# Optimization experiments

Hardware: AMD Instinct MI355X
Metric: run time of the kernel (lower is better)

## Reference

```python
import math
import jax, jax.numpy as jnp
import numpy as np

B, T, C, FD, K, V = 8, 2048, 256, 256, 128, 256

def setup_inputs() -> dict:
    key = jax.random.key(0)
    ks = jax.random.split(key, 8)
    s = 0.02
    return {
        "inp": jax.random.normal(ks[0], (B, T, C), jnp.float32),
        "feature": jax.random.normal(ks[1], (B, T, FD), jnp.float32),
        "Wq": jax.random.normal(ks[2], (C + FD, K), jnp.float32) * s,
        "bq": jnp.zeros((K,), jnp.float32),
        "Wk": jax.random.normal(ks[3], (C, K), jnp.float32) * s,
        "bk": jnp.zeros((K,), jnp.float32),
        "Wv": jax.random.normal(ks[4], (C, V), jnp.float32) * s,
        "bv": jnp.zeros((V,), jnp.float32),
    }

def reference(inp, feature, Wq, bq, Wk, bk, Wv, bv):
    # inp: [B,T,C], feature: [B,T,FD]
    t = inp.shape[1]
    q = jnp.concatenate([inp, feature], axis=-1) @ Wq + bq   # [B,T,K]
    k = inp @ Wk + bk                                        # [B,T,K]
    v = inp @ Wv + bv                                        # [B,T,V]
    # scores[b, j, i] = q_j . k_i ; original masks where i > j (strict upper tri)
    scores = jnp.einsum('bjk,bik->bji', q, k)                # [B,T,T]
    mask = jnp.triu(jnp.ones((t, t), dtype=bool), k=1)       # mask[j,i] = i > j
    scores = jnp.where(mask[None], -jnp.inf, scores) / math.sqrt(K)
    # NOTE: original softmax is over dim=1 (the query/row axis), not the key axis
    attn = jax.nn.softmax(scores, axis=1)                    # [B,T,T]
    out = jnp.einsum('bji,biv->bjv', attn, v)                # [B,T,V]
    return jnp.concatenate([inp, out], axis=-1)              # [B,T,C+V]
```

## Files before the change

### kernel.cpp

```cpp
#include <hip/hip_runtime.h>
#include <hip/hip_bf16.h>
#include <cstdint>

#define Bb  8
#define Tt  2048
#define Cc  256
#define FDd 256
#define Kk  128
#define Vv  256
#define BT  (Bb * Tt)
#define NTRI 136

#define INV_SQRT_K 0.08838834764831845f

typedef __bf16 bf16x8 __attribute__((ext_vector_type(8)));
typedef __bf16 bf16x4 __attribute__((ext_vector_type(4)));
typedef float  f32x4  __attribute__((ext_vector_type(4)));

__device__ __forceinline__ void gload16(const void* g, void* l) {
  __builtin_amdgcn_global_load_lds(
      (const __attribute__((address_space(1))) void*)g,
      (__attribute__((address_space(3))) void*)l, 16, 0, 0);
}

__global__ __launch_bounds__(256) void prep_kernel(
    const float4* __restrict__ inp4, const float4* __restrict__ feat4,
    float4* __restrict__ out4, bf16x4* __restrict__ inpB4,
    bf16x4* __restrict__ featB4)
{
  const int g = blockIdx.x * 256 + threadIdx.x;
  const int row = g >> 6, c = g & 63;
  const float4 x = inp4[g];
  out4[(size_t)row * 128 + c] = x;
  bf16x4 xb; xb[0] = (__bf16)x.x; xb[1] = (__bf16)x.y; xb[2] = (__bf16)x.z; xb[3] = (__bf16)x.w;
  inpB4[g] = xb;
  const float4 f = feat4[g];
  bf16x4 fb; fb[0] = (__bf16)f.x; fb[1] = (__bf16)f.y; fb[2] = (__bf16)f.z; fb[3] = (__bf16)f.w;
  featB4[g] = fb;
}

__global__ __launch_bounds__(256) void wprep_kernel(
    const float* __restrict__ Wq, const float* __restrict__ Wk,
    const float* __restrict__ Wv, __bf16* __restrict__ Wqt,
    __bf16* __restrict__ Wkt, __bf16* __restrict__ Wvt)
{
  const int g = blockIdx.x * 256 + threadIdx.x;
  if (g < 65536) {
    const int n = g >> 9, k = g & 511;
    Wqt[g] = (__bf16)Wq[k * 128 + n];
  } else if (g < 98304) {
    const int h = g - 65536;
    const int n = h >> 8, k = h & 255;
    Wkt[h] = (__bf16)Wk[k * 128 + n];
  } else {
    const int h = g - 98304;
    const int n = h >> 8, k = h & 255;
    Wvt[h] = (__bf16)Wv[k * 256 + n];
  }
}

__global__ __launch_bounds__(256, 3) void qkv_mfma_kernel(
    const __bf16* __restrict__ inpB, const __bf16* __restrict__ featB,
    const __bf16* __restrict__ Wqt, const __bf16* __restrict__ Wkt,
    const __bf16* __restrict__ Wvt,
    const float* __restrict__ bq, const float* __restrict__ bk,
    const float* __restrict__ bv,
    __bf16* __restrict__ qb, __bf16* __restrict__ kb, __bf16* __restrict__ vT)
{
  __shared__ __bf16 Atile[128 * 64];
  __shared__ __bf16 Btile[128 * 64];
  const int panel = blockIdx.y;
  const int m0 = blockIdx.x * 128;
  const int lane = threadIdx.x & 63, wave = threadIdx.x >> 6;
  const int cl = lane & 15, quad = lane >> 4;
  const int jl0 = (wave >> 1) * 64;
  const int vl0 = (wave & 1) * 64;

  const __bf16* Wt; const float* bias; int kblocks;
  if (panel == 0)      { Wt = Wqt; bias = bq; kblocks = 8; }
  else if (panel == 1) { Wt = Wkt; bias = bk; kblocks = 4; }
  else                 { Wt = Wvt + (size_t)(panel - 2) * 128 * 256;
                         bias = bv + (panel - 2) * 128; kblocks = 4; }
  const int Kd = kblocks * 64;

  const int lrow = lane >> 3;
  const int lchunk = ((lane & 7) ^ lrow) * 8;

  f32x4 acc[4][4];
#pragma unroll
  for (int mt = 0; mt < 4; ++mt)
#pragma unroll
    for (int nt = 0; nt < 4; ++nt) acc[mt][nt] = (f32x4){0.f, 0.f, 0.f, 0.f};

  for (int kb = 0; kb < kblocks; ++kb) {
    const __bf16* Asrc = (panel == 0 && kb >= 4) ? featB : inpB;
    const int koff = (panel == 0 && kb >= 4) ? (kb - 4) * 64 : kb * 64;
    __syncthreads();
#pragma unroll
    for (int t = 0; t < 4; ++t) {
      const int r0 = wave * 32 + t * 8;
      gload16(Asrc + (size_t)(m0 + r0 + lrow) * 256 + koff + lchunk, Atile + r0 * 64);
      gload16(Wt + (size_t)(r0 + lrow) * Kd + kb * 64 + lchunk, Btile + r0 * 64);
    }
    __syncthreads();
#pragma unroll
    for (int ks = 0; ks < 2; ++ks) {
      bf16x8 af[4], bfr[4];
#pragma unroll
      for (int mt = 0; mt < 4; ++mt) {
        const int jlr = jl0 + mt * 16 + cl;
        af[mt] = *(const bf16x8*)(Atile + jlr * 64 + (((ks * 4 + quad) ^ (jlr & 7)) * 8));
      }
#pragma unroll
      for (int nt = 0; nt < 4; ++nt) {
        const int vlr = vl0 + nt * 16 + cl;
        bfr[nt] = *(const bf16x8*)(Btile + vlr * 64 + (((ks * 4 + quad) ^ (vlr & 7)) * 8));
      }
#pragma unroll
      for (int mt = 0; mt < 4; ++mt)
#pragma unroll
        for (int nt = 0; nt < 4; ++nt)
          acc[mt][nt] = __builtin_amdgcn_mfma_f32_16x16x32_bf16(af[mt], bfr[nt], acc[mt][nt], 0, 0, 0);
    }
  }

  if (panel < 2) {
    __bf16* dst = (panel == 0) ? qb : kb;
    const float scale = (panel == 0) ? INV_SQRT_K : 1.0f;
#pragma unroll
    for (int mt = 0; mt < 4; ++mt) {
      const int row = m0 + jl0 + mt * 16 + quad * 4;
#pragma unroll
      for (int nt = 0; nt < 4; ++nt) {
        const int col = vl0 + nt * 16 + cl;
        const float bs = bias[col];
#pragma unroll
        for (int r = 0; r < 4; ++r)
          dst[(size_t)(row + r) * Kk + col] = (__bf16)((acc[mt][nt][r] + bs) * scale);
      }
    }
  } else {
    const int b = m0 >> 11;
#pragma unroll
    for (int mt = 0; mt < 4; ++mt) {
      const int t0 = (m0 & (Tt - 1)) + jl0 + mt * 16 + quad * 4;
#pragma unroll
      for (int nt = 0; nt < 4; ++nt) {
        const int vcol = (panel - 2) * 128 + vl0 + nt * 16 + cl;
        const float bs = bias[vl0 + nt * 16 + cl];
        bf16x4 v4;
#pragma unroll
        for (int r = 0; r < 4; ++r) v4[r] = (__bf16)(acc[mt][nt][r] + bs);
        *(bf16x4*)(vT + (size_t)(b * Vv + vcol) * Tt + t0) = v4;
      }
    }
  }
}

__global__ __launch_bounds__(256, 2) void sexp_kernel(
    const __bf16* __restrict__ qb, const __bf16* __restrict__ kb,
    __bf16* __restrict__ expS, float* __restrict__ partialD)
{
  __shared__ __bf16 tiles[2 * 128 * 128];
  __shared__ float lcs[4][64];
  __bf16* Qtile = tiles;
  __bf16* Ktile = tiles + 128 * 128;
  float*  P     = (float*)tiles;

  const int b = blockIdx.y, l = blockIdx.x;
  int jt = 0, base = 0;
  while (base + jt + 1 <= l) { base += jt + 1; ++jt; }
  const int it = l - base;

  const int lane = threadIdx.x & 63, wave = threadIdx.x >> 6;
  const int cl = lane & 15, quad = lane >> 4;
  const int jl0 = (wave >> 1) * 64;
  const int il0 = (wave & 1) * 64;
  const size_t rowbase = (size_t)b * Tt;

  {
    const int srow = lane >> 4;
    const int cslot = lane & 15;
    const __bf16* qsrc = qb + (rowbase + jt * 128) * Kk;
    const __bf16* ksrc = kb + (rowbase + it * 128) * Kk;
#pragma unroll
    for (int t = 0; t < 8; ++t) {
      const int r0 = wave * 32 + t * 4;
      const int row = r0 + srow;
      const int cg = (cslot ^ (row & 7)) * 8;
      gload16(qsrc + (size_t)row * Kk + cg, Qtile + r0 * 128);
      gload16(ksrc + (size_t)row * Kk + cg, Ktile + r0 * 128);
    }
  }
  __syncthreads();

  f32x4 acc[4][4];
#pragma unroll
  for (int mt = 0; mt < 4; ++mt)
#pragma unroll
    for (int nt = 0; nt < 4; ++nt) acc[mt][nt] = (f32x4){0.f, 0.f, 0.f, 0.f};

#pragma unroll
  for (int s = 0; s < 4; ++s) {
    bf16x8 af[4], bfr[4];
#pragma unroll
    for (int mt = 0; mt < 4; ++mt) {
      const int jlr = jl0 + mt * 16 + cl;
      af[mt] = *(const bf16x8*)(Qtile + jlr * 128 + (((s * 4 + quad) ^ (jlr & 7)) * 8));
    }
#pragma unroll
    for (int nt = 0; nt < 4; ++nt) {
      const int ilr = il0 + nt * 16 + cl;
      bfr[nt] = *(const bf16x8*)(Ktile + ilr * 128 + (((s * 4 + quad) ^ (ilr & 7)) * 8));
    }
#pragma unroll
    for (int mt = 0; mt < 4; ++mt)
#pragma unroll
      for (int nt = 0; nt < 4; ++nt)
        acc[mt][nt] = __builtin_amdgcn_mfma_f32_16x16x32_bf16(af[mt], bfr[nt], acc[mt][nt], 0, 0, 0);
  }
  __syncthreads();

  const bool diag = (it == jt);
  float cs[4] = {0.f, 0.f, 0.f, 0.f};
#pragma unroll
  for (int mt = 0; mt < 4; ++mt) {
    const int jl = jl0 + mt * 16 + quad * 4;
#pragma unroll
    for (int nt = 0; nt < 4; ++nt) {
      const int il = il0 + nt * 16 + cl;
#pragma unroll
      for (int r = 0; r < 4; ++r) {
        float p = __expf(acc[mt][nt][r]);
        if (diag && il > (jl + r)) p = 0.f;
        cs[nt] += (float)(__bf16)p;
        P[(jl + r) * 128 + il] = p;
      }
    }
  }
#pragma unroll
  for (int nt = 0; nt < 4; ++nt) {
    cs[nt] += __shfl_xor(cs[nt], 16);
    cs[nt] += __shfl_xor(cs[nt], 32);
  }
  if (quad == 0) {
#pragma unroll
    for (int nt = 0; nt < 4; ++nt) lcs[wave][nt * 16 + cl] = cs[nt];
  }
  __syncthreads();

  __bf16* slot = expS + ((size_t)(b * NTRI + l)) * (128 * 128);
  {
    const int srow = lane >> 4;
    const int c0 = (lane & 15) * 8;
#pragma unroll
    for (int t = 0; t < 8; ++t) {
      const int row = wave * 32 + t * 4 + srow;
      const f32x4 p0 = *(const f32x4*)(P + row * 128 + c0);
      const f32x4 p1 = *(const f32x4*)(P + row * 128 + c0 + 4);
      bf16x8 pb;
#pragma unroll
      for (int u = 0; u < 4; ++u) { pb[u] = (__bf16)p0[u]; pb[4 + u] = (__bf16)p1[u]; }
      *(bf16x8*)(slot + (size_t)row * 128 + c0) = pb;
    }
  }

  const int tid = threadIdx.x;
  if (tid < 128) {
    const int w0 = (tid < 64) ? 0 : 1;
    const int lc = tid & 63;
    const float s = lcs[w0][lc] + lcs[w0 + 2][lc];
    partialD[((size_t)b * 16 + jt) * Tt + it * 128 + tid] = s;
  }
}

__global__ __launch_bounds__(256) void dreduce_kernel(
    const float* __restrict__ partialD, float* __restrict__ recipD)
{
  const int g = blockIdx.x * 256 + threadIdx.x;
  const int b = g >> 11, i = g & (Tt - 1);
  float s = 0.f;
#pragma unroll
  for (int jt = 0; jt < 16; ++jt) s += partialD[((size_t)b * 16 + jt) * Tt + i];
  recipD[g] = 1.0f / s;
}

__global__ __launch_bounds__(256) void vscale_kernel(
    bf16x8* __restrict__ vT8, const float* __restrict__ recipD)
{
  const int g = blockIdx.x * 256 + threadIdx.x;
  const size_t e0 = (size_t)g * 8;
  const int i = (int)(e0 & (Tt - 1));
  const int b = (int)(e0 >> 19);
  bf16x8 v = vT8[g];
  const f32x4 r0 = *(const f32x4*)(recipD + (size_t)b * Tt + i);
  const f32x4 r1 = *(const f32x4*)(recipD + (size_t)b * Tt + i + 4);
#pragma unroll
  for (int t = 0; t < 4; ++t) v[t] = (__bf16)((float)v[t] * r0[t]);
#pragma unroll
  for (int t = 0; t < 4; ++t) v[4 + t] = (__bf16)((float)v[4 + t] * r1[t]);
  vT8[g] = v;
}

__global__ __launch_bounds__(256, 3) void pvgemm_kernel(
    const __bf16* __restrict__ expS, const __bf16* __restrict__ vT,
    float* __restrict__ out)
{
  __shared__ __bf16 Atile[128 * 64];
  __shared__ __bf16 Btile[128 * 64];
  const int b = blockIdx.y;
  const int jt = 15 - (blockIdx.x >> 1);
  const int nh = blockIdx.x & 1;
  const int lane = threadIdx.x & 63, wave = threadIdx.x >> 6;
  const int cl = lane & 15, quad = lane >> 4;
  const int jl0 = (wave >> 1) * 64;
  const int vl0 = (wave & 1) * 64;

  const int kblocks = (jt + 1) * 2;
  const size_t slotbase = (size_t)(b * NTRI + (jt * (jt + 1)) / 2) * 16384;
  const __bf16* vbase = vT + ((size_t)b * Vv + nh * 128) * Tt;

  const int lrow = lane >> 3;
  const int lchunk = ((lane & 7) ^ lrow) * 8;

  f32x4 acc[4][4];
#pragma unroll
  for (int mt = 0; mt < 4; ++mt)
#pragma unroll
    for (int nt = 0; nt < 4; ++nt) acc[mt][nt] = (f32x4){0.f, 0.f, 0.f, 0.f};

  for (int kb = 0; kb < kblocks; ++kb) {
    const int i0 = kb * 64;
    const __bf16* Ag = expS + slotbase + (size_t)(kb >> 1) * 16384 + (kb & 1) * 64;
    __syncthreads();
#pragma unroll
    for (int t = 0; t < 4; ++t) {
      const int r0 = wave * 32 + t * 8;
      gload16(Ag + (size_t)(r0 + lrow) * 128 + lchunk, Atile + r0 * 64);
      gload16(vbase + (size_t)(r0 + lrow) * Tt + i0 + lchunk, Btile + r0 * 64);
    }
    __syncthreads();
#pragma unroll
    for (int ks = 0; ks < 2; ++ks) {
      bf16x8 af[4], bfr[4];
#pragma unroll
      for (int mt = 0; mt < 4; ++mt) {
        const int jlr = jl0 + mt * 16 + cl;
        af[mt] = *(const bf16x8*)(Atile + jlr * 64 + (((ks * 4 + quad) ^ (jlr & 7)) * 8));
      }
#pragma unroll
      for (int nt = 0; nt < 4; ++nt) {
        const int vlr = vl0 + nt * 16 + cl;
        bfr[nt] = *(const bf16x8*)(Btile + vlr * 64 + (((ks * 4 + quad) ^ (vlr & 7)) * 8));
      }
#pragma unroll
      for (int mt = 0; mt < 4; ++mt)
#pragma unroll
        for (int nt = 0; nt < 4; ++nt)
          acc[mt][nt] = __builtin_amdgcn_mfma_f32_16x16x32_bf16(af[mt], bfr[nt], acc[mt][nt], 0, 0, 0);
    }
  }

  float* orow = out + ((size_t)b * Tt + jt * 128 + jl0) * (size_t)(Cc + Vv)
              + Cc + nh * 128 + vl0;
#pragma unroll
  for (int mt = 0; mt < 4; ++mt)
#pragma unroll
    for (int nt = 0; nt < 4; ++nt)
#pragma unroll
      for (int r = 0; r < 4; ++r)
        orow[(size_t)(mt * 16 + quad * 4 + r) * (Cc + Vv) + nt * 16 + cl] = acc[mt][nt][r];
}

extern "C" void kernel_launch(void* const* d_in, const int* in_sizes, int n_in,
                              void* d_out, int out_size, void* d_ws, size_t ws_size,
                              hipStream_t stream) {
  const float* inp  = (const float*)d_in[0];
  const float* feat = (const float*)d_in[1];
  const float* Wq   = (const float*)d_in[2];
  const float* bq   = (const float*)d_in[3];
  const float* Wk   = (const float*)d_in[4];
  const float* bk   = (const float*)d_in[5];
  const float* Wv   = (const float*)d_in[6];
  const float* bv   = (const float*)d_in[7];
  float* out = (float*)d_out;

  char* ws = (char*)d_ws;
  __bf16* inpB   = (__bf16*)(ws);
  __bf16* featB  = (__bf16*)(ws + (8u << 20));
  __bf16* qb     = (__bf16*)(ws + (16u << 20));
  __bf16* kb     = (__bf16*)(ws + (20u << 20));
  __bf16* vT     = (__bf16*)(ws + (24u << 20));
  __bf16* Wqt    = (__bf16*)(ws + (32u << 20));
  __bf16* Wkt    = (__bf16*)(ws + (32u << 20) + (128u << 10));
  __bf16* Wvt    = (__bf16*)(ws + (32u << 20) + (192u << 10));
  float*  partialD = (float*)(ws + (33u << 20));
  float*  recipD   = (float*)(ws + (35u << 20));
  __bf16* expS     = (__bf16*)(ws + (36u << 20));

  prep_kernel<<<dim3(BT * 64 / 256), 256, 0, stream>>>(
      (const float4*)inp, (const float4*)feat, (float4*)out,
      (bf16x4*)inpB, (bf16x4*)featB);
  wprep_kernel<<<dim3(640), 256, 0, stream>>>(Wq, Wk, Wv, Wqt, Wkt, Wvt);
  qkv_mfma_kernel<<<dim3(BT / 128, 4), 256, 0, stream>>>(
      inpB, featB, Wqt, Wkt, Wvt, bq, bk, bv, qb, kb, vT);
  sexp_kernel<<<dim3(NTRI, Bb), 256, 0, stream>>>(qb, kb, expS, partialD);
  dreduce_kernel<<<dim3(BT / 256), 256, 0, stream>>>(partialD, recipD);
  vscale_kernel<<<dim3(2048), 256, 0, stream>>>((bf16x8*)vT, recipD);
  pvgemm_kernel<<<dim3(32, Bb), 256, 0, stream>>>(expS, vT, out);
}
```

Baseline: 173.0 us.

## Split-K the PV GEMM across two wave groups and merge small launches

The PV GEMM now runs 512 threads per block. Two groups of four waves each take half of the K range into separate LDS buffers, and their partial sums are combined through a shared reduction buffer before the output is written. The prep and weight-transpose kernels are merged into one launch, and the column-sum reduction is fused with the V scaling, removing two launches and the recipD round trip. This targets launch overhead and the load imbalance of the triangular PV work, at the cost of extra LDS (about 96KB per block) and an additional synchronisation and reduction step.

```diff
diff --git a/kernel.cpp b/kernel.cpp
--- a/kernel.cpp
+++ b/kernel.cpp
@@ -23,39 +23,38 @@
       (__attribute__((address_space(3))) void*)l, 16, 0, 0);
 }
 
-__global__ __launch_bounds__(256) void prep_kernel(
+__global__ __launch_bounds__(256) void prepw_kernel(
     const float4* __restrict__ inp4, const float4* __restrict__ feat4,
     float4* __restrict__ out4, bf16x4* __restrict__ inpB4,
-    bf16x4* __restrict__ featB4)
-{
-  const int g = blockIdx.x * 256 + threadIdx.x;
-  const int row = g >> 6, c = g & 63;
-  const float4 x = inp4[g];
-  out4[(size_t)row * 128 + c] = x;
-  bf16x4 xb; xb[0] = (__bf16)x.x; xb[1] = (__bf16)x.y; xb[2] = (__bf16)x.z; xb[3] = (__bf16)x.w;
-  inpB4[g] = xb;
-  const float4 f = feat4[g];
-  bf16x4 fb; fb[0] = (__bf16)f.x; fb[1] = (__bf16)f.y; fb[2] = (__bf16)f.z; fb[3] = (__bf16)f.w;
-  featB4[g] = fb;
-}
-
-__global__ __launch_bounds__(256) void wprep_kernel(
+    bf16x4* __restrict__ featB4,
     const float* __restrict__ Wq, const float* __restrict__ Wk,
     const float* __restrict__ Wv, __bf16* __restrict__ Wqt,
     __bf16* __restrict__ Wkt, __bf16* __restrict__ Wvt)
 {
-  const int g = blockIdx.x * 256 + threadIdx.x;
-  if (g < 65536) {
-    const int n = g >> 9, k = g & 511;
-    Wqt[g] = (__bf16)Wq[k * 128 + n];
-  } else if (g < 98304) {
-    const int h = g - 65536;
-    const int n = h >> 8, k = h & 255;
-    Wkt[h] = (__bf16)Wk[k * 128 + n];
+  if (blockIdx.x < 4096) {
+    const int g = blockIdx.x * 256 + threadIdx.x;
+    const int row = g >> 6, c = g & 63;
+    const float4 x = inp4[g];
+    out4[(size_t)row * 128 + c] = x;
+    bf16x4 xb; xb[0] = (__bf16)x.x; xb[1] = (__bf16)x.y; xb[2] = (__bf16)x.z; xb[3] = (__bf16)x.w;
+    inpB4[g] = xb;
+    const float4 f = feat4[g];
+    bf16x4 fb; fb[0] = (__bf16)f.x; fb[1] = (__bf16)f.y; fb[2] = (__bf16)f.z; fb[3] = (__bf16)f.w;
+    featB4[g] = fb;
   } else {
-    const int h = g - 98304;
-    const int n = h >> 8, k = h & 255;
-    Wvt[h] = (__bf16)Wv[k * 256 + n];
+    const int g = (blockIdx.x - 4096) * 256 + threadIdx.x;
+    if (g < 65536) {
+      const int n = g >> 9, k = g & 511;
+      Wqt[g] = (__bf16)Wq[k * 128 + n];
+    } else if (g < 98304) {
+      const int h = g - 65536;
+      const int n = h >> 8, k = h & 255;
+      Wkt[h] = (__bf16)Wk[k * 128 + n];
+    } else {
+      const int h = g - 98304;
+      const int n = h >> 8, k = h & 255;
+      Wvt[h] = (__bf16)Wv[k * 256 + n];
+    }
   }
 }
 
@@ -274,49 +273,55 @@
   }
 }
 
-__global__ __launch_bounds__(256) void dreduce_kernel(
-    const float* __restrict__ partialD, float* __restrict__ recipD)
+__global__ __launch_bounds__(256) void dvscale_kernel(
+    const float* __restrict__ partialD, bf16x8* __restrict__ vT8)
 {
-  const int g = blockIdx.x * 256 + threadIdx.x;
-  const int b = g >> 11, i = g & (Tt - 1);
-  float s = 0.f;
-#pragma unroll
-  for (int jt = 0; jt < 16; ++jt) s += partialD[((size_t)b * 16 + jt) * Tt + i];
-  recipD[g] = 1.0f / s;
-}
-
-__global__ __launch_bounds__(256) void vscale_kernel(
-    bf16x8* __restrict__ vT8, const float* __restrict__ recipD)
-{
-  const int g = blockIdx.x * 256 + threadIdx.x;
-  const size_t e0 = (size_t)g * 8;
-  const int i = (int)(e0 & (Tt - 1));
-  const int b = (int)(e0 >> 19);
-  bf16x8 v = vT8[g];
-  const f32x4 r0 = *(const f32x4*)(recipD + (size_t)b * Tt + i);
-  const f32x4 r1 = *(const f32x4*)(recipD + (size_t)b * Tt + i + 4);
-#pragma unroll
-  for (int t = 0; t < 4; ++t) v[t] = (__bf16)((float)v[t] * r0[t]);
-#pragma unroll
-  for (int t = 0; t < 4; ++t) v[4 + t] = (__bf16)((float)v[4 + t] * r1[t]);
-  vT8[g] = v;
-}
-
-__global__ __launch_bounds__(256, 3) void pvgemm_kernel(
+  __shared__ float rec[32];
+  const int blk = blockIdx.x;
+  const int b = blk >> 6, ic = blk & 63;
+  const int i0 = ic * 32;
+  const int tid = threadIdx.x;
+  if (tid < 32) {
+    const int i = i0 + tid;
+    float s = 0.f;
+#pragma unroll
+    for (int jt = 0; jt < 16; ++jt) s += partialD[((size_t)b * 16 + jt) * Tt + i];
+    rec[tid] = 1.0f / s;
+  }
+  __syncthreads();
+  const int iu = tid & 3, v0 = tid >> 2;
+#pragma unroll
+  for (int p = 0; p < 4; ++p) {
+    const int v = v0 + p * 64;
+    const size_t idx = ((size_t)b * Vv + v) * (Tt / 8) + (i0 >> 3) + iu;
+    bf16x8 x = vT8[idx];
+    const int rb = iu * 8;
+#pragma unroll
+    for (int t = 0; t < 8; ++t) x[t] = (__bf16)((float)x[t] * rec[rb + t]);
+    vT8[idx] = x;
+  }
+}
+
+__global__ __launch_bounds__(512, 2) void pvgemm_kernel(
     const __bf16* __restrict__ expS, const __bf16* __restrict__ vT,
     float* __restrict__ out)
 {
-  __shared__ __bf16 Atile[128 * 64];
-  __shared__ __bf16 Btile[128 * 64];
+  __shared__ __bf16 At[2][128 * 64];
+  __shared__ __bf16 Bt[2][128 * 64];
+  __shared__ float red[4][16][256];
   const int b = blockIdx.y;
   const int jt = 15 - (blockIdx.x >> 1);
   const int nh = blockIdx.x & 1;
-  const int lane = threadIdx.x & 63, wave = threadIdx.x >> 6;
+  const int tid = (int)threadIdx.x;
+  const int lane = tid & 63, wave = tid >> 6;
+  const int kh = wave >> 2;
+  const int sq = wave & 3;
   const int cl = lane & 15, quad = lane >> 4;
-  const int jl0 = (wave >> 1) * 64;
-  const int vl0 = (wave & 1) * 64;
-
-  const int kblocks = (jt + 1) * 2;
+  const int jl0 = (sq >> 1) * 64;
+  const int vl0 = (sq & 1) * 64;
+
+  const int nk = (jt + 1) * 2;
+  const int half = nk >> 1;
   const size_t slotbase = (size_t)(b * NTRI + (jt * (jt + 1)) / 2) * 16384;
   const __bf16* vbase = vT + ((size_t)b * Vv + nh * 128) * Tt;
 
@@ -329,15 +334,16 @@
 #pragma unroll
     for (int nt = 0; nt < 4; ++nt) acc[mt][nt] = (f32x4){0.f, 0.f, 0.f, 0.f};
 
-  for (int kb = 0; kb < kblocks; ++kb) {
+  for (int kbl = 0; kbl < half; ++kbl) {
+    const int kb = kh * half + kbl;
     const int i0 = kb * 64;
     const __bf16* Ag = expS + slotbase + (size_t)(kb >> 1) * 16384 + (kb & 1) * 64;
     __syncthreads();
 #pragma unroll
     for (int t = 0; t < 4; ++t) {
-      const int r0 = wave * 32 + t * 8;
-      gload16(Ag + (size_t)(r0 + lrow) * 128 + lchunk, Atile + r0 * 64);
-      gload16(vbase + (size_t)(r0 + lrow) * Tt + i0 + lchunk, Btile + r0 * 64);
+      const int r0 = sq * 32 + t * 8;
+      gload16(Ag + (size_t)(r0 + lrow) * 128 + lchunk, At[kh] + r0 * 64);
+      gload16(vbase + (size_t)(r0 + lrow) * Tt + i0 + lchunk, Bt[kh] + r0 * 64);
     }
     __syncthreads();
 #pragma unroll
@@ -346,12 +352,12 @@
 #pragma unroll
       for (int mt = 0; mt < 4; ++mt) {
         const int jlr = jl0 + mt * 16 + cl;
-        af[mt] = *(const bf16x8*)(Atile + jlr * 64 + (((ks * 4 + quad) ^ (jlr & 7)) * 8));
+        af[mt] = *(const bf16x8*)(At[kh] + jlr * 64 + (((ks * 4 + quad) ^ (jlr & 7)) * 8));
       }
 #pragma unroll
       for (int nt = 0; nt < 4; ++nt) {
         const int vlr = vl0 + nt * 16 + cl;
-        bfr[nt] = *(const bf16x8*)(Btile + vlr * 64 + (((ks * 4 + quad) ^ (vlr & 7)) * 8));
+        bfr[nt] = *(const bf16x8*)(Bt[kh] + vlr * 64 + (((ks * 4 + quad) ^ (vlr & 7)) * 8));
       }
 #pragma unroll
       for (int mt = 0; mt < 4; ++mt)
@@ -361,15 +367,33 @@
     }
   }
 
-  float* orow = out + ((size_t)b * Tt + jt * 128 + jl0) * (size_t)(Cc + Vv)
-              + Cc + nh * 128 + vl0;
-#pragma unroll
-  for (int mt = 0; mt < 4; ++mt)
-#pragma unroll
-    for (int nt = 0; nt < 4; ++nt)
-#pragma unroll
-      for (int r = 0; r < 4; ++r)
-        orow[(size_t)(mt * 16 + quad * 4 + r) * (Cc + Vv) + nt * 16 + cl] = acc[mt][nt][r];
+  __syncthreads();
+  if (kh == 1) {
+#pragma unroll
+    for (int mt = 0; mt < 4; ++mt)
+#pragma unroll
+      for (int nt = 0; nt < 4; ++nt)
+        *(f32x4*)&red[sq][mt * 4 + nt][lane * 4] = acc[mt][nt];
+  }
+  __syncthreads();
+  if (kh == 0) {
+#pragma unroll
+    for (int mt = 0; mt < 4; ++mt)
+#pragma unroll
+      for (int nt = 0; nt < 4; ++nt) {
+        const f32x4 o = *(const f32x4*)&red[sq][mt * 4 + nt][lane * 4];
+        acc[mt][nt] += o;
+      }
+    float* orow = out + ((size_t)b * Tt + jt * 128 + jl0) * (size_t)(Cc + Vv)
+                + Cc + nh * 128 + vl0;
+#pragma unroll
+    for (int mt = 0; mt < 4; ++mt)
+#pragma unroll
+      for (int nt = 0; nt < 4; ++nt)
+#pragma unroll
+        for (int r = 0; r < 4; ++r)
+          orow[(size_t)(mt * 16 + quad * 4 + r) * (Cc + Vv) + nt * 16 + cl] = acc[mt][nt][r];
+  }
 }
 
 extern "C" void kernel_launch(void* const* d_in, const int* in_sizes, int n_in,
@@ -395,17 +419,14 @@
   __bf16* Wkt    = (__bf16*)(ws + (32u << 20) + (128u << 10));
   __bf16* Wvt    = (__bf16*)(ws + (32u << 20) + (192u << 10));
   float*  partialD = (float*)(ws + (33u << 20));
-  float*  recipD   = (float*)(ws + (35u << 20));
   __bf16* expS     = (__bf16*)(ws + (36u << 20));
 
-  prep_kernel<<<dim3(BT * 64 / 256), 256, 0, stream>>>(
+  prepw_kernel<<<dim3(4096 + 640), 256, 0, stream>>>(
       (const float4*)inp, (const float4*)feat, (float4*)out,
-      (bf16x4*)inpB, (bf16x4*)featB);
-  wprep_kernel<<<dim3(640), 256, 0, stream>>>(Wq, Wk, Wv, Wqt, Wkt, Wvt);
+      (bf16x4*)inpB, (bf16x4*)featB, Wq, Wk, Wv, Wqt, Wkt, Wvt);
   qkv_mfma_kernel<<<dim3(BT / 128, 4), 256, 0, stream>>>(
       inpB, featB, Wqt, Wkt, Wvt, bq, bk, bv, qb, kb, vT);
   sexp_kernel<<<dim3(NTRI, Bb), 256, 0, stream>>>(qb, kb, expS, partialD);
-  dreduce_kernel<<<dim3(BT / 256), 256, 0, stream>>>(partialD, recipD);
-  vscale_kernel<<<dim3(2048), 256, 0, stream>>>((bf16x8*)vT, recipD);
-  pvgemm_kernel<<<dim3(32, Bb), 256, 0, stream>>>(expS, vT, out);
-}
+  dvscale_kernel<<<dim3(512), 256, 0, stream>>>(partialD, (bf16x8*)vT);
+  pvgemm_kernel<<<dim3(32, Bb), 512, 0, stream>>>(expS, vT, out);
+}
```

After: 170.5 us. No clear change (-1.5%).
